# Performance work log

Hardware: AMD Instinct MI355X
Metric: run time of the kernel (lower is better)

Reference implementation:

```python
import jax, jax.numpy as jnp
import numpy as np
from jax import lax

STRIDE = 2
PADDING = 3
NUM_ROW = 8192
NUM_COL = 8192
KH, KW = 7, 7


def setup_inputs() -> dict:
    key = jax.random.key(0)
    kx, kw_, kb = jax.random.split(key, 3)
    enc_x = jax.random.normal(kx, (NUM_ROW * NUM_COL,), dtype=jnp.float32)
    weight = jax.random.normal(kw_, (1, 1, KH, KW), dtype=jnp.float32)
    bias = jax.random.normal(kb, (1,), dtype=jnp.float32)
    return {
        "enc_x": enc_x,
        "weight": weight,
        "bias": bias,
        "num_row": NUM_ROW,
        "num_col": NUM_COL,
    }


def reference(enc_x, weight, bias, num_row, num_col):
    # enc_x is the flattened (packed) image vector of a num_row x num_col image.
    # The CKKS Conv2dFunction computes a plain single-channel cross-correlation
    # (same semantics as torch Conv2d, 1 in / 1 out channel) + scalar bias,
    # returning the flattened output vector.
    x = enc_x.reshape(1, 1, num_row, num_col)  # NCHW
    out = lax.conv_general_dilated(
        x,
        weight,  # OIHW
        window_strides=(STRIDE, STRIDE),
        padding=[(PADDING, PADDING), (PADDING, PADDING)],
        dimension_numbers=("NCHW", "OIHW", "NCHW"),
    )
    out = out + bias[0]
    return out.reshape(-1)  # flattened, matching ciphertext packing
```

## Files before the change

### kernel.cpp

```cpp
#include <hip/hip_runtime.h>


#define THREADS 256
#define TILE_W 256
#define TILE_H 8
#define IN_H 21
#define CHUNKS 130
#define ROWF (CHUNKS * 4)
#define NSLOT (IN_H * CHUNKS)
#define NROUND 11
#define NSLOT_PAD (NROUND * THREADS)
#define IMG 8192
#define OUTW 4096
#define GRIDX 16

typedef float __attribute__((ext_vector_type(4))) floatx4;

__global__ __launch_bounds__(THREADS, 3)
void conv7x7_s2(const float* __restrict__ x, const float* __restrict__ wgt,
                const float* __restrict__ bias, float* __restrict__ out) {
  __shared__ __align__(16) float lds[NSLOT_PAD * 4];
  const int t = threadIdx.x;

  const int bid = blockIdx.x + GRIDX * blockIdx.y;
  const int xcd = bid & 7;
  const int local = bid >> 3;
  const int bx = 2 * xcd + (local >> 9);
  const int by = local & 511;

  const int tile_x = bx * TILE_W;
  const int tile_y = by * TILE_H;
  const int g0c4 = tile_x * 2 - 4;
  const int g0r = tile_y * 2 - 3;

  float wv[49];
#pragma unroll
  for (int i = 0; i < 49; ++i) wv[i] = wgt[i];
  const float bv = bias[0];

  const bool interior = (bx >= 1) & (bx <= 14) & (by >= 1) & (by <= 510);

  float4 vbuf[NROUND];
  if (interior) {
    const float* xb = x + (long long)g0r * IMG + g0c4;
#pragma unroll
    for (int i = 0; i < NROUND; ++i) {
      const int s = t + THREADS * i;
      if (s < NSLOT) {
        const int r = s / CHUNKS;
        const int g = s - r * CHUNKS;
        vbuf[i] = *reinterpret_cast<const float4*>(xb + (long long)r * IMG + 4 * g);
      }
    }
  } else {
#pragma unroll
    for (int i = 0; i < NROUND; ++i) {
      const int s = t + THREADS * i;
      const int r = s / CHUNKS;
      const int g = s - r * CHUNKS;
      const int gr = g0r + r;
      const int gc = g0c4 + 4 * g;
      float4 v = make_float4(0.f, 0.f, 0.f, 0.f);
      if (s < NSLOT && (unsigned)gr < (unsigned)IMG &&
          (unsigned)gc < (unsigned)(IMG - 3))
        v = *reinterpret_cast<const float4*>(&x[(long long)gr * IMG + gc]);
      vbuf[i] = v;
    }
  }
#pragma unroll
  for (int i = 0; i < NROUND; ++i) {
    const int s = t + THREADS * i;
    if (s < NSLOT) {
      const int r = s / CHUNKS;
      const int g = s - r * CHUNKS;
      const int sl = (g & 1) ? (65 + (g >> 1)) : (g >> 1);
      *reinterpret_cast<float4*>(&lds[(r * CHUNKS + sl) * 4]) = vbuf[i];
    }
  }
  __syncthreads();

  const int tx = t & 63;
  const int ty = t >> 6;
  float acc[2][4];
#pragma unroll
  for (int y = 0; y < 2; ++y)
#pragma unroll
    for (int xx = 0; xx < 4; ++xx) acc[y][xx] = bv;

#pragma unroll
  for (int j = 0; j < 9; ++j) {
    const int sl = 4 * ty + j;
    const float* rp = &lds[sl * ROWF];
    float rbuf[16];
    {
      const float4 v0 = *reinterpret_cast<const float4*>(rp + (tx) * 4);
      const float4 v1 = *reinterpret_cast<const float4*>(rp + (65 + tx) * 4);
      const float4 v2 = *reinterpret_cast<const float4*>(rp + (tx + 1) * 4);
      const float4 v3 = *reinterpret_cast<const float4*>(rp + (66 + tx) * 4);
      rbuf[0] = v0.x;  rbuf[1] = v0.y;  rbuf[2] = v0.z;  rbuf[3] = v0.w;
      rbuf[4] = v1.x;  rbuf[5] = v1.y;  rbuf[6] = v1.z;  rbuf[7] = v1.w;
      rbuf[8] = v2.x;  rbuf[9] = v2.y;  rbuf[10] = v2.z; rbuf[11] = v2.w;
      rbuf[12] = v3.x; rbuf[13] = v3.y; rbuf[14] = v3.z; rbuf[15] = v3.w;
    }
#pragma unroll
    for (int y = 0; y < 2; ++y) {
      const int kh = j - 2 * y;
      if (kh >= 0 && kh <= 6) {
#pragma unroll
        for (int xx = 0; xx < 4; ++xx)
#pragma unroll
          for (int kw = 0; kw < 7; ++kw)
            acc[y][xx] = fmaf(rbuf[2 * xx + kw + 1], wv[kh * 7 + kw], acc[y][xx]);
      }
    }
  }

  const int ox = tile_x + 4 * tx;
  const int oy = tile_y + 2 * ty;
#pragma unroll
  for (int y = 0; y < 2; ++y) {
    floatx4 v;
    v.x = acc[y][0]; v.y = acc[y][1]; v.z = acc[y][2]; v.w = acc[y][3];
    __builtin_nontemporal_store(
        v, reinterpret_cast<floatx4*>(&out[(long long)(oy + y) * OUTW + ox]));
  }
}

extern "C" void kernel_launch(void* const* d_in, const int* in_sizes, int n_in,
                              void* d_out, int out_size, void* d_ws, size_t ws_size,
                              hipStream_t stream) {
  const float* x = (const float*)d_in[0];
  const float* w = (const float*)d_in[1];
  const float* b = (const float*)d_in[2];
  float* out = (float*)d_out;
  dim3 grid(GRIDX, OUTW / TILE_H);
  conv7x7_s2<<<grid, dim3(THREADS), 0, stream>>>(x, w, b, out);
}
```

Baseline: 59.43 us.

## Process two row tiles per block with register prefetch of next tile

Each block now computes two consecutive 8-row output tiles, prefetching the second tile's input into registers while computing the first, then rewriting LDS after a barrier. This aims to overlap global load latency with FMA work and amortize weight loads and block setup. It adds barriers, halves the grid, and raises register pressure from the live prefetch buffer, which may reduce occupancy.

```diff
diff --git a/kernel.cpp b/kernel.cpp
--- a/kernel.cpp
+++ b/kernel.cpp
@@ -3,7 +3,6 @@
 
 #define THREADS 256
 #define TILE_W 256
-#define TILE_H 8
 #define IN_H 21
 #define CHUNKS 130
 #define ROWF (CHUNKS * 4)
@@ -13,6 +12,7 @@
 #define IMG 8192
 #define OUTW 4096
 #define GRIDX 16
+#define GRIDY 256
 
 typedef float __attribute__((ext_vector_type(4))) floatx4;
 
@@ -25,74 +25,82 @@
   const int bid = blockIdx.x + GRIDX * blockIdx.y;
   const int xcd = bid & 7;
   const int local = bid >> 3;
-  const int bx = 2 * xcd + (local >> 9);
-  const int by = local & 511;
+  const int bx = 2 * xcd + (local >> 8);
+  const int byp = local & 255;
 
   const int tile_x = bx * TILE_W;
-  const int tile_y = by * TILE_H;
+  const int tile_y0 = byp * 16;
   const int g0c4 = tile_x * 2 - 4;
-  const int g0r = tile_y * 2 - 3;
+  const int g0rA = tile_y0 * 2 - 3;
 
   float wv[49];
 #pragma unroll
   for (int i = 0; i < 49; ++i) wv[i] = wgt[i];
   const float bv = bias[0];
 
-  const bool interior = (bx >= 1) & (bx <= 14) & (by >= 1) & (by <= 510);
+  const bool interior = (bx >= 1) & (bx <= 14) & (byp >= 1) & (byp <= 254);
+
+  int s_r[NROUND], s_g[NROUND];
+#pragma unroll
+  for (int i = 0; i < NROUND; ++i) {
+    const int s = t + THREADS * i;
+    s_r[i] = s / CHUNKS;
+    s_g[i] = s - s_r[i] * CHUNKS;
+  }
 
   float4 vbuf[NROUND];
-  if (interior) {
-    const float* xb = x + (long long)g0r * IMG + g0c4;
+
+  auto LOAD = [&](int g0r) {
+    if (interior) {
+      const float* xb = x + (long long)g0r * IMG + g0c4;
+#pragma unroll
+      for (int i = 0; i < NROUND; ++i) {
+        if (t + THREADS * i < NSLOT)
+          vbuf[i] = *reinterpret_cast<const float4*>(
+              xb + (long long)s_r[i] * IMG + 4 * s_g[i]);
+      }
+    } else {
+#pragma unroll
+      for (int i = 0; i < NROUND; ++i) {
+        const int s = t + THREADS * i;
+        const int gr = g0r + s_r[i];
+        const int gc = g0c4 + 4 * s_g[i];
+        float4 v = make_float4(0.f, 0.f, 0.f, 0.f);
+        if (s < NSLOT && (unsigned)gr < (unsigned)IMG &&
+            (unsigned)gc < (unsigned)(IMG - 3))
+          v = *reinterpret_cast<const float4*>(&x[(long long)gr * IMG + gc]);
+        vbuf[i] = v;
+      }
+    }
+  };
+
+  auto WRITE = [&]() {
 #pragma unroll
     for (int i = 0; i < NROUND; ++i) {
       const int s = t + THREADS * i;
       if (s < NSLOT) {
-        const int r = s / CHUNKS;
-        const int g = s - r * CHUNKS;
-        vbuf[i] = *reinterpret_cast<const float4*>(xb + (long long)r * IMG + 4 * g);
+        const int g = s_g[i];
+        const int sl = (g & 1) ? (65 + (g >> 1)) : (g >> 1);
+        *reinterpret_cast<float4*>(&lds[(s_r[i] * CHUNKS + sl) * 4]) = vbuf[i];
       }
     }
-  } else {
-#pragma unroll
-    for (int i = 0; i < NROUND; ++i) {
-      const int s = t + THREADS * i;
-      const int r = s / CHUNKS;
-      const int g = s - r * CHUNKS;
-      const int gr = g0r + r;
-      const int gc = g0c4 + 4 * g;
-      float4 v = make_float4(0.f, 0.f, 0.f, 0.f);
-      if (s < NSLOT && (unsigned)gr < (unsigned)IMG &&
-          (unsigned)gc < (unsigned)(IMG - 3))
-        v = *reinterpret_cast<const float4*>(&x[(long long)gr * IMG + gc]);
-      vbuf[i] = v;
-    }
-  }
-#pragma unroll
-  for (int i = 0; i < NROUND; ++i) {
-    const int s = t + THREADS * i;
-    if (s < NSLOT) {
-      const int r = s / CHUNKS;
-      const int g = s - r * CHUNKS;
-      const int sl = (g & 1) ? (65 + (g >> 1)) : (g >> 1);
-      *reinterpret_cast<float4*>(&lds[(r * CHUNKS + sl) * 4]) = vbuf[i];
-    }
-  }
-  __syncthreads();
+  };
 
   const int tx = t & 63;
   const int ty = t >> 6;
-  float acc[2][4];
+
+  auto COMPUTE_STORE = [&](int sub) {
+    float acc[2][4];
 #pragma unroll
-  for (int y = 0; y < 2; ++y)
+    for (int y = 0; y < 2; ++y)
 #pragma unroll
-    for (int xx = 0; xx < 4; ++xx) acc[y][xx] = bv;
+      for (int xx = 0; xx < 4; ++xx) acc[y][xx] = bv;
 
 #pragma unroll
-  for (int j = 0; j < 9; ++j) {
-    const int sl = 4 * ty + j;
-    const float* rp = &lds[sl * ROWF];
-    float rbuf[16];
-    {
+    for (int j = 0; j < 9; ++j) {
+      const int sl = 4 * ty + j;
+      const float* rp = &lds[sl * ROWF];
+      float rbuf[16];
       const float4 v0 = *reinterpret_cast<const float4*>(rp + (tx) * 4);
       const float4 v1 = *reinterpret_cast<const float4*>(rp + (65 + tx) * 4);
       const float4 v2 = *reinterpret_cast<const float4*>(rp + (tx + 1) * 4);
@@ -101,29 +109,39 @@
       rbuf[4] = v1.x;  rbuf[5] = v1.y;  rbuf[6] = v1.z;  rbuf[7] = v1.w;
       rbuf[8] = v2.x;  rbuf[9] = v2.y;  rbuf[10] = v2.z; rbuf[11] = v2.w;
       rbuf[12] = v3.x; rbuf[13] = v3.y; rbuf[14] = v3.z; rbuf[15] = v3.w;
+#pragma unroll
+      for (int y = 0; y < 2; ++y) {
+        const int kh = j - 2 * y;
+        if (kh >= 0 && kh <= 6) {
+#pragma unroll
+          for (int xx = 0; xx < 4; ++xx)
+#pragma unroll
+            for (int kw = 0; kw < 7; ++kw)
+              acc[y][xx] = fmaf(rbuf[2 * xx + kw + 1], wv[kh * 7 + kw], acc[y][xx]);
+        }
+      }
     }
+    const int ox = tile_x + 4 * tx;
+    const int oy = tile_y0 + 8 * sub + 2 * ty;
 #pragma unroll
     for (int y = 0; y < 2; ++y) {
-      const int kh = j - 2 * y;
-      if (kh >= 0 && kh <= 6) {
-#pragma unroll
-        for (int xx = 0; xx < 4; ++xx)
-#pragma unroll
-          for (int kw = 0; kw < 7; ++kw)
-            acc[y][xx] = fmaf(rbuf[2 * xx + kw + 1], wv[kh * 7 + kw], acc[y][xx]);
-      }
+      floatx4 v;
+      v.x = acc[y][0]; v.y = acc[y][1]; v.z = acc[y][2]; v.w = acc[y][3];
+      __builtin_nontemporal_store(
+          v, reinterpret_cast<floatx4*>(&out[(long long)(oy + y) * OUTW + ox]));
     }
-  }
+  };
 
-  const int ox = tile_x + 4 * tx;
-  const int oy = tile_y + 2 * ty;
-#pragma unroll
-  for (int y = 0; y < 2; ++y) {
-    floatx4 v;
-    v.x = acc[y][0]; v.y = acc[y][1]; v.z = acc[y][2]; v.w = acc[y][3];
-    __builtin_nontemporal_store(
-        v, reinterpret_cast<floatx4*>(&out[(long long)(oy + y) * OUTW + ox]));
-  }
+  LOAD(g0rA);
+  WRITE();
+  __syncthreads();
+
+  LOAD(g0rA + 16);
+  COMPUTE_STORE(0);
+  __syncthreads();
+  WRITE();
+  __syncthreads();
+  COMPUTE_STORE(1);
 }
 
 extern "C" void kernel_launch(void* const* d_in, const int* in_sizes, int n_in,
@@ -133,6 +151,6 @@
   const float* w = (const float*)d_in[1];
   const float* b = (const float*)d_in[2];
   float* out = (float*)d_out;
-  dim3 grid(GRIDX, OUTW / TILE_H);
+  dim3 grid(GRIDX, GRIDY);
   conv7x7_s2<<<grid, dim3(THREADS), 0, stream>>>(x, w, b, out);
 }
```

After: 126.6 us. 113% more time.
